# Optimization experiments

Measured on AMD Instinct MI355X. Metric: run time of the kernel, lower is better.

Reference implementation:

```python
import jax, jax.numpy as jnp
import numpy as np

N_NODES = 100_000
N_EDGES = 1_600_000
D = 128  # in = hidden = out channels
LAYERS = 3


def setup_inputs() -> dict:
    key = jax.random.key(0)
    ks = jax.random.split(key, 16)
    inp = {
        "x": jax.random.normal(ks[0], (N_NODES, D), dtype=jnp.float32),
        "edge_weight": jax.random.uniform(ks[1], (N_EDGES,), dtype=jnp.float32),
    }
    scale = 1.0 / np.sqrt(D)
    for l in range(LAYERS):
        inp[f"W_rel_{l}"] = jax.random.normal(ks[2 + 3 * l], (D, D), dtype=jnp.float32) * scale
        inp[f"W_root_{l}"] = jax.random.normal(ks[3 + 3 * l], (D, D), dtype=jnp.float32) * scale
        inp[f"b_{l}"] = jax.random.normal(ks[4 + 3 * l], (D,), dtype=jnp.float32) * scale
    inp["edge_src"] = jax.random.randint(ks[11], (N_EDGES,), 0, N_NODES, dtype=jnp.int32)
    inp["edge_dst"] = jax.random.randint(ks[12], (N_EDGES,), 0, N_NODES, dtype=jnp.int32)
    return inp


def _graph_conv(h, edge_src, edge_dst, edge_weight, W_rel, W_root, b):
    # PyG GraphConv: out_i = W_root @ h_i + W_rel @ (sum_{j->i} w_ji * h_j) + b
    msg = h[edge_src] * edge_weight[:, None]                      # [E, D] gather
    agg = jax.ops.segment_sum(msg, edge_dst, num_segments=h.shape[0])  # [N, D] scatter-add
    return agg @ W_rel.T + h @ W_root.T + b


def reference(x, edge_weight, W_rel_0, W_root_0, b_0, W_rel_1, W_root_1, b_1,
              W_rel_2, W_root_2, b_2, edge_src, edge_dst):
    h = _graph_conv(x, edge_src, edge_dst, edge_weight, W_rel_0, W_root_0, b_0)
    h = jax.nn.relu(h)
    h = _graph_conv(h, edge_src, edge_dst, edge_weight, W_rel_1, W_root_1, b_1)
    h = jax.nn.relu(h)
    h = _graph_conv(h, edge_src, edge_dst, edge_weight, W_rel_2, W_root_2, b_2)
    return h
```

## Files before the change

### kernel.cpp

```cpp
#include <hip/hip_runtime.h>

#define N_NODES 100000
#define N_EDGES 1600000
#define D 128
#define GEMM_GRID 3125
#define BK_NODES 256
#define N_BUCKETS 391
#define BKT_CAP 5120
#define SC_BLOCKS 128
#define EPB 12500

typedef _Float16 f16;
typedef _Float16 f16x8 __attribute__((ext_vector_type(8)));
typedef _Float16 f16x2 __attribute__((ext_vector_type(2)));
typedef float f32x2 __attribute__((ext_vector_type(2)));
typedef float f32x4 __attribute__((ext_vector_type(4)));

__device__ __forceinline__ unsigned bf16bits(float x) {
    unsigned u = __float_as_uint(x);
    return ((u + 0x8000u) >> 16) & 0x7fffu;
}


__global__ __launch_bounds__(256) void bucket_scatter(const int* __restrict__ src,
                                                      const int* __restrict__ dst,
                                                      const float* __restrict__ w,
                                                      int* __restrict__ bcur,
                                                      int2* __restrict__ bkt) {
    __shared__ int hist[N_BUCKETS];
    __shared__ int base[N_BUCKETS];
    int tid = threadIdx.x;
    int v0  = blockIdx.x * (EPB / 4);
    const int4*   dst4 = (const int4*)dst;
    const int4*   src4 = (const int4*)src;
    const float4* w4   = (const float4*)w;

    for (int b = tid; b < N_BUCKETS; b += 256) hist[b] = 0;
    __syncthreads();

    for (int v = tid; v < EPB / 4; v += 256) {
        int4 d = dst4[v0 + v];
        atomicAdd(&hist[d.x >> 8], 1);
        atomicAdd(&hist[d.y >> 8], 1);
        atomicAdd(&hist[d.z >> 8], 1);
        atomicAdd(&hist[d.w >> 8], 1);
    }
    __syncthreads();

    for (int b = tid; b < N_BUCKETS; b += 256) {
        int c = hist[b];
        base[b] = b * BKT_CAP + ((c > 0) ? atomicAdd(&bcur[b], c) : 0);
        hist[b] = 0;
    }
    __syncthreads();

    for (int v = tid; v < EPB / 4; v += 256) {
        int4   d = dst4[v0 + v];
        int4   s = src4[v0 + v];
        float4 f = w4[v0 + v];
        {
            int p = base[d.x >> 8] + atomicAdd(&hist[d.x >> 8], 1);
            bkt[p] = make_int2(s.x, (int)(((unsigned)d.x << 15) | bf16bits(f.x)));
        }
        {
            int p = base[d.y >> 8] + atomicAdd(&hist[d.y >> 8], 1);
            bkt[p] = make_int2(s.y, (int)(((unsigned)d.y << 15) | bf16bits(f.y)));
        }
        {
            int p = base[d.z >> 8] + atomicAdd(&hist[d.z >> 8], 1);
            bkt[p] = make_int2(s.z, (int)(((unsigned)d.z << 15) | bf16bits(f.z)));
        }
        {
            int p = base[d.w >> 8] + atomicAdd(&hist[d.w >> 8], 1);
            bkt[p] = make_int2(s.w, (int)(((unsigned)d.w << 15) | bf16bits(f.w)));
        }
    }
}

__global__ __launch_bounds__(512) void bucket_scan(const int* __restrict__ bcnt,
                                                   int* __restrict__ bbase) {
    __shared__ int sc[512];
    int tid = threadIdx.x;
    int v = (tid < N_BUCKETS) ? bcnt[tid] : 0;
    sc[tid] = v;
    __syncthreads();
    for (int off = 1; off < 512; off <<= 1) {
        int t = (tid >= off) ? sc[tid - off] : 0;
        __syncthreads();
        sc[tid] += t;
        __syncthreads();
    }
    if (tid < N_BUCKETS) bbase[tid] = sc[tid] - v;
}

__global__ __launch_bounds__(256) void bucket_finalize(const int* __restrict__ bcnt,
                                                       const int* __restrict__ bbase,
                                                       const int2* __restrict__ bkt,
                                                       unsigned* __restrict__ csr,
                                                       int* __restrict__ row_ptr) {
    __shared__ int ncnt[BK_NODES];
    __shared__ int noff[BK_NODES];
    __shared__ int sc[BK_NODES];
    int tid   = threadIdx.x;
    int b     = blockIdx.x;
    int node0 = b * BK_NODES;
    int cnt   = bcnt[b];
    int base  = bbase[b];
    int e0    = b * BKT_CAP;

    ncnt[tid] = 0;
    __syncthreads();
    for (int i = tid; i < cnt; i += 256) {
        int local = (int)((unsigned)bkt[e0 + i].y >> 15) - node0;
        atomicAdd(&ncnt[local], 1);
    }
    __syncthreads();
    int s = ncnt[tid];
    sc[tid] = s;
    __syncthreads();
    for (int off = 1; off < 256; off <<= 1) {
        int t = (tid >= off) ? sc[tid - off] : 0;
        __syncthreads();
        sc[tid] += t;
        __syncthreads();
    }
    noff[tid] = sc[tid] - s;
    ncnt[tid] = 0;
    {
        int nN = N_NODES - node0; if (nN > BK_NODES) nN = BK_NODES;
        if (tid < nN) row_ptr[node0 + tid] = base + noff[tid];
        if (b == N_BUCKETS - 1 && tid == 0) row_ptr[N_NODES] = N_EDGES;
    }
    __syncthreads();
    for (int i = tid; i < cnt; i += 256) {
        int2 t = bkt[e0 + i];
        unsigned meta = (unsigned)t.y;
        int local = (int)(meta >> 15) - node0;
        int p = base + noff[local] + atomicAdd(&ncnt[local], 1);
        csr[p] = ((unsigned)t.x << 15) | (meta & 0x7fffu);
    }
}


__global__ __launch_bounds__(256) void cvt_x(const float* __restrict__ in,
                                             f16* __restrict__ out16,
                                             unsigned char* __restrict__ out8) {
    int i = blockIdx.x * 256 + threadIdx.x;
    const float4* in4 = (const float4*)in;
    float4 a = in4[i * 2], b = in4[i * 2 + 1];
    f16x8 v;
    v[0] = (f16)a.x; v[1] = (f16)a.y; v[2] = (f16)a.z; v[3] = (f16)a.w;
    v[4] = (f16)b.x; v[5] = (f16)b.y; v[6] = (f16)b.z; v[7] = (f16)b.w;
    ((f16x8*)out16)[i] = v;
    uint2 p8;
    int r = __builtin_amdgcn_cvt_pk_fp8_f32(a.x, a.y, 0, false);
    r     = __builtin_amdgcn_cvt_pk_fp8_f32(a.z, a.w, r, true);
    p8.x = (unsigned)r;
    r     = __builtin_amdgcn_cvt_pk_fp8_f32(b.x, b.y, 0, false);
    r     = __builtin_amdgcn_cvt_pk_fp8_f32(b.z, b.w, r, true);
    p8.y = (unsigned)r;
    ((uint2*)out8)[i] = p8;
}


__global__ __launch_bounds__(256) void pack_weights(const float* __restrict__ Wrel,
                                                    const float* __restrict__ Wroot,
                                                    f16* __restrict__ Bp) {
    int idx = blockIdx.x * 256 + threadIdx.x;
    int e = idx & 7, lane = (idx >> 3) & 63, ct = (idx >> 9) & 7, ks = idx >> 12;
    int j = ct * 16 + (lane & 15);
    int k = ks * 32 + (lane >> 4) * 8 + e;
    float w = (k < D) ? Wrel[j * D + k] : Wroot[j * D + (k - D)];
    Bp[idx] = (f16)w;
}


#define FMA8(CWV)                                                              \
    {                                                                          \
        float w = __uint_as_float(((CWV) & 0x7fffu) << 16);                    \
        f32x2 c0 = __builtin_amdgcn_cvt_pk_f32_fp8((int)rv[j].x, false);       \
        f32x2 c1 = __builtin_amdgcn_cvt_pk_f32_fp8((int)rv[j].x, true);        \
        f32x2 c2 = __builtin_amdgcn_cvt_pk_f32_fp8((int)rv[j].y, false);       \
        f32x2 c3 = __builtin_amdgcn_cvt_pk_f32_fp8((int)rv[j].y, true);        \
        a0 = fmaf(w, c0.x, a0); a1 = fmaf(w, c0.y, a1);                        \
        a2 = fmaf(w, c1.x, a2); a3 = fmaf(w, c1.y, a3);                        \
        a4 = fmaf(w, c2.x, a4); a5 = fmaf(w, c2.y, a5);                        \
        a6 = fmaf(w, c3.x, a6); a7 = fmaf(w, c3.y, a7);                        \
    }

template <int FINAL>
__global__ __launch_bounds__(256) void fused_layer(const f16* __restrict__ h,
                                                   const unsigned char* __restrict__ h8,
                                                   const int* __restrict__ row_ptr,
                                                   const unsigned* __restrict__ csr,
                                                   const f16x8* __restrict__ Bp,
                                                   const float* __restrict__ bias,
                                                   void* __restrict__ outp,
                                                   unsigned char* __restrict__ outp8) {
    __shared__ f16 sA[32 * 256];
    int tid  = threadIdx.x;
    int lane = tid & 63;
    int wid  = tid >> 6;
    int node0 = blockIdx.x * 32;
    const uint4* h16 = (const uint4*)h;

    int quad = lane >> 4;
    int ql   = lane & 15;
    unsigned qoff = (unsigned)ql * 8u;

    for (int nn = 0; nn < 2; ++nn) {
        int row  = wid * 8 + quad * 2 + nn;
        int node = node0 + row;
        int beg = row_ptr[node], end = row_ptr[node + 1];

        float a0 = 0.f, a1 = 0.f, a2 = 0.f, a3 = 0.f;
        float a4 = 0.f, a5 = 0.f, a6 = 0.f, a7 = 0.f;

        int e = beg;
        unsigned cw[8];
        if (e + 8 <= end) {
#pragma unroll
            for (int j = 0; j < 8; ++j) cw[j] = csr[e + j];
        }
        while (e + 8 <= end) {
            uint2 rv[8];
            __builtin_amdgcn_sched_barrier(0);
#pragma unroll
            for (int j = 0; j < 8; ++j) {
                unsigned off = ((cw[j] >> 8) & 0xFFFFFF80u) | qoff;
                rv[j] = *(const uint2*)(h8 + off);
            }
            unsigned cwn[8];
            bool more = (e + 16 <= end);
            if (more) {
#pragma unroll
                for (int j = 0; j < 8; ++j) cwn[j] = csr[e + 8 + j];
            }
            __builtin_amdgcn_sched_barrier(0);
#pragma unroll
            for (int j = 0; j < 8; ++j) FMA8(cw[j]);
            if (more) {
#pragma unroll
                for (int j = 0; j < 8; ++j) cw[j] = cwn[j];
            }
            e += 8;
        }
        if (e < end) {
            int rem = end - e;
            int em1 = end - 1;
            unsigned sm[8];
            uint2 rv[8];
#pragma unroll
            for (int j = 0; j < 8; ++j) {
                int idx = e + j; idx = idx < em1 ? idx : em1;
                unsigned c = csr[idx];
                sm[j] = (j < rem) ? c : 0u;
            }
            __builtin_amdgcn_sched_barrier(0);
#pragma unroll
            for (int j = 0; j < 8; ++j) {
                unsigned off = ((sm[j] >> 8) & 0xFFFFFF80u) | qoff;
                rv[j] = *(const uint2*)(h8 + off);
            }
            __builtin_amdgcn_sched_barrier(0);
#pragma unroll
            for (int j = 0; j < 8; ++j) FMA8(sm[j]);
        }
        f16x8 ov;
        ov[0] = (f16)a0; ov[1] = (f16)a1; ov[2] = (f16)a2; ov[3] = (f16)a3;
        ov[4] = (f16)a4; ov[5] = (f16)a5; ov[6] = (f16)a6; ov[7] = (f16)a7;
        int o = (row * 256 + ql * 8) ^ ((row & 7) << 3);
        *(f16x8*)&sA[o] = ov;
    }

#pragma unroll
    for (int it = 0; it < 2; ++it) {
        int i = it * 256 + tid, r = i >> 4, c8 = (i & 15) + 16;
        int o = (r * 256 + c8 * 8) ^ ((r & 7) << 3);
        *(uint4*)&sA[o] = h16[(size_t)(node0 + r) * 16 + (c8 - 16)];
    }
    __syncthreads();

    int wrow = wid >> 1;
    int wcol = wid & 1;
    float bv[4];
#pragma unroll
    for (int c = 0; c < 4; ++c) bv[c] = bias[wcol * 64 + c * 16 + (lane & 15)];

    f32x4 acc[4] = {f32x4{0,0,0,0}, f32x4{0,0,0,0}, f32x4{0,0,0,0}, f32x4{0,0,0,0}};
    int arow = wrow * 16 + (lane & 15);
    int kg   = (lane >> 4) * 8;

    f16x8 b0 = Bp[(0 * 8 + wcol * 4 + 0) * 64 + lane];
    f16x8 b1 = Bp[(0 * 8 + wcol * 4 + 1) * 64 + lane];
    f16x8 b2 = Bp[(0 * 8 + wcol * 4 + 2) * 64 + lane];
    f16x8 b3 = Bp[(0 * 8 + wcol * 4 + 3) * 64 + lane];
#pragma unroll 1
    for (int ks = 0; ks < 8; ++ks) {
        f16x8 n0, n1, n2, n3;
        if (ks < 7) {
            n0 = Bp[((ks + 1) * 8 + wcol * 4 + 0) * 64 + lane];
            n1 = Bp[((ks + 1) * 8 + wcol * 4 + 1) * 64 + lane];
            n2 = Bp[((ks + 1) * 8 + wcol * 4 + 2) * 64 + lane];
            n3 = Bp[((ks + 1) * 8 + wcol * 4 + 3) * 64 + lane];
        }
        int o = (arow * 256 + ks * 32 + kg) ^ ((arow & 7) << 3);
        f16x8 afrag = *(const f16x8*)&sA[o];
        acc[0] = __builtin_amdgcn_mfma_f32_16x16x32_f16(afrag, b0, acc[0], 0, 0, 0);
        acc[1] = __builtin_amdgcn_mfma_f32_16x16x32_f16(afrag, b1, acc[1], 0, 0, 0);
        acc[2] = __builtin_amdgcn_mfma_f32_16x16x32_f16(afrag, b2, acc[2], 0, 0, 0);
        acc[3] = __builtin_amdgcn_mfma_f32_16x16x32_f16(afrag, b3, acc[3], 0, 0, 0);
        b0 = n0; b1 = n1; b2 = n2; b3 = n3;
    }

#pragma unroll
    for (int c = 0; c < 4; ++c) {
        int col = wcol * 64 + c * 16 + (lane & 15);
#pragma unroll
        for (int r = 0; r < 4; ++r) {
            int row = node0 + wrow * 16 + (lane >> 4) * 4 + r;
            float o = acc[c][r] + bv[c];
            if (FINAL) {
                ((float*)outp)[(size_t)row * D + col] = o;
            } else {
                o = fmaxf(o, 0.f);
                ((f16*)outp)[(size_t)row * D + col] = (f16)o;
                int pk = __builtin_amdgcn_cvt_pk_fp8_f32(o, o, 0, false);
                outp8[(size_t)row * D + col] = (unsigned char)(pk & 0xff);
            }
        }
    }
}


extern "C" void kernel_launch(void* const* d_in, const int* in_sizes, int n_in,
                              void* d_out, int out_size, void* d_ws, size_t ws_size,
                              hipStream_t stream) {
    const float* x  = (const float*)d_in[0];
    const float* ew = (const float*)d_in[1];
    const float* W_rel[3]  = {(const float*)d_in[2], (const float*)d_in[5], (const float*)d_in[8]};
    const float* W_root[3] = {(const float*)d_in[3], (const float*)d_in[6], (const float*)d_in[9]};
    const float* bias[3]   = {(const float*)d_in[4], (const float*)d_in[7], (const float*)d_in[10]};
    const int* esrc = (const int*)d_in[11];
    const int* edst = (const int*)d_in[12];

    char* ws = (char*)d_ws;
    f16*           bufA16  = (f16*)           (ws);
    unsigned char* bufA8   = (unsigned char*) (ws + 25600000);
    f16*           bufB16  = (f16*)           (ws + 38400000);
    unsigned char* bufB8   = (unsigned char*) (ws + 64000000);
    unsigned*      csr     = (unsigned*)      (ws + 76800000);
    int2*          bkt     = (int2*)          (ws + 83200000);
    int*           row_ptr = (int*)           (ws + 99215360);
    int*           bcur    = (int*)           (ws + 99615376);
    int*           bbase   = (int*)           (ws + 99616940);
    f16*           Bp      = (f16*)           (ws + 99618504);

    hipMemsetAsync(bcur, 0, N_BUCKETS * sizeof(int), stream);
    bucket_scatter<<<SC_BLOCKS, 256, 0, stream>>>(esrc, edst, ew, bcur, bkt);
    bucket_scan<<<1, 512, 0, stream>>>(bcur, bbase);
    bucket_finalize<<<N_BUCKETS, 256, 0, stream>>>(bcur, bbase, bkt, csr, row_ptr);

    cvt_x<<<6250, 256, 0, stream>>>(x, bufA16, bufA8);
    for (int l = 0; l < 3; ++l)
        pack_weights<<<128, 256, 0, stream>>>(W_rel[l], W_root[l], Bp + l * 32768);

    fused_layer<0><<<GEMM_GRID, 256, 0, stream>>>(bufA16, bufA8, row_ptr, csr,
                                                  (const f16x8*)(Bp + 0 * 32768),
                                                  bias[0], bufB16, bufB8);
    fused_layer<0><<<GEMM_GRID, 256, 0, stream>>>(bufB16, bufB8, row_ptr, csr,
                                                  (const f16x8*)(Bp + 1 * 32768),
                                                  bias[1], bufA16, bufA8);
    fused_layer<1><<<GEMM_GRID, 256, 0, stream>>>(bufA16, bufA8, row_ptr, csr,
                                                  (const f16x8*)(Bp + 2 * 32768),
                                                  bias[2], d_out, nullptr);
}
```

Baseline: 226.9 us.

## Halve fused layer tile to 16 nodes per block, doubling grid

```diff
diff --git a/kernel.cpp b/kernel.cpp
--- a/kernel.cpp
+++ b/kernel.cpp
@@ -3,7 +3,8 @@
 #define N_NODES 100000
 #define N_EDGES 1600000
 #define D 128
-#define GEMM_GRID 3125
+#define GEMM_GRID 6250
+#define TILE_ROWS 16
 #define BK_NODES 256
 #define N_BUCKETS 391
 #define BKT_CAP 5120
@@ -197,19 +198,19 @@
                                                    const float* __restrict__ bias,
                                                    void* __restrict__ outp,
                                                    unsigned char* __restrict__ outp8) {
-    __shared__ f16 sA[32 * 256];
+    __shared__ f16 sA[TILE_ROWS * 256];
     int tid  = threadIdx.x;
     int lane = tid & 63;
     int wid  = tid >> 6;
-    int node0 = blockIdx.x * 32;
+    int node0 = blockIdx.x * TILE_ROWS;
     const uint4* h16 = (const uint4*)h;
 
     int quad = lane >> 4;
     int ql   = lane & 15;
     unsigned qoff = (unsigned)ql * 8u;
 
-    for (int nn = 0; nn < 2; ++nn) {
-        int row  = wid * 8 + quad * 2 + nn;
+    {
+        int row  = wid * 4 + quad;
         int node = node0 + row;
         int beg = row_ptr[node], end = row_ptr[node + 1];
 
@@ -273,52 +274,43 @@
         *(f16x8*)&sA[o] = ov;
     }
 
-#pragma unroll
-    for (int it = 0; it < 2; ++it) {
-        int i = it * 256 + tid, r = i >> 4, c8 = (i & 15) + 16;
+    {
+        int r = tid >> 4, c8 = (tid & 15) + 16;
         int o = (r * 256 + c8 * 8) ^ ((r & 7) << 3);
         *(uint4*)&sA[o] = h16[(size_t)(node0 + r) * 16 + (c8 - 16)];
     }
     __syncthreads();
 
-    int wrow = wid >> 1;
-    int wcol = wid & 1;
-    float bv[4];
-#pragma unroll
-    for (int c = 0; c < 4; ++c) bv[c] = bias[wcol * 64 + c * 16 + (lane & 15)];
-
-    f32x4 acc[4] = {f32x4{0,0,0,0}, f32x4{0,0,0,0}, f32x4{0,0,0,0}, f32x4{0,0,0,0}};
-    int arow = wrow * 16 + (lane & 15);
+    float bv[2];
+#pragma unroll
+    for (int c = 0; c < 2; ++c) bv[c] = bias[wid * 32 + c * 16 + (lane & 15)];
+
+    f32x4 acc[2] = {f32x4{0,0,0,0}, f32x4{0,0,0,0}};
+    int arow = lane & 15;
     int kg   = (lane >> 4) * 8;
 
-    f16x8 b0 = Bp[(0 * 8 + wcol * 4 + 0) * 64 + lane];
-    f16x8 b1 = Bp[(0 * 8 + wcol * 4 + 1) * 64 + lane];
-    f16x8 b2 = Bp[(0 * 8 + wcol * 4 + 2) * 64 + lane];
-    f16x8 b3 = Bp[(0 * 8 + wcol * 4 + 3) * 64 + lane];
+    f16x8 b0 = Bp[(0 * 8 + wid * 2 + 0) * 64 + lane];
+    f16x8 b1 = Bp[(0 * 8 + wid * 2 + 1) * 64 + lane];
 #pragma unroll 1
     for (int ks = 0; ks < 8; ++ks) {
-        f16x8 n0, n1, n2, n3;
+        f16x8 n0, n1;
         if (ks < 7) {
-            n0 = Bp[((ks + 1) * 8 + wcol * 4 + 0) * 64 + lane];
-            n1 = Bp[((ks + 1) * 8 + wcol * 4 + 1) * 64 + lane];
-            n2 = Bp[((ks + 1) * 8 + wcol * 4 + 2) * 64 + lane];
-            n3 = Bp[((ks + 1) * 8 + wcol * 4 + 3) * 64 + lane];
+            n0 = Bp[((ks + 1) * 8 + wid * 2 + 0) * 64 + lane];
+            n1 = Bp[((ks + 1) * 8 + wid * 2 + 1) * 64 + lane];
         }
         int o = (arow * 256 + ks * 32 + kg) ^ ((arow & 7) << 3);
         f16x8 afrag = *(const f16x8*)&sA[o];
         acc[0] = __builtin_amdgcn_mfma_f32_16x16x32_f16(afrag, b0, acc[0], 0, 0, 0);
         acc[1] = __builtin_amdgcn_mfma_f32_16x16x32_f16(afrag, b1, acc[1], 0, 0, 0);
-        acc[2] = __builtin_amdgcn_mfma_f32_16x16x32_f16(afrag, b2, acc[2], 0, 0, 0);
-        acc[3] = __builtin_amdgcn_mfma_f32_16x16x32_f16(afrag, b3, acc[3], 0, 0, 0);
-        b0 = n0; b1 = n1; b2 = n2; b3 = n3;
-    }
-
-#pragma unroll
-    for (int c = 0; c < 4; ++c) {
-        int col = wcol * 64 + c * 16 + (lane & 15);
+        b0 = n0; b1 = n1;
+    }
+
+#pragma unroll
+    for (int c = 0; c < 2; ++c) {
+        int col = wid * 32 + c * 16 + (lane & 15);
 #pragma unroll
         for (int r = 0; r < 4; ++r) {
-            int row = node0 + wrow * 16 + (lane >> 4) * 4 + r;
+            int row = node0 + (lane >> 4) * 4 + r;
             float o = acc[c][r] + bv[c];
             if (FINAL) {
                 ((float*)outp)[(size_t)row * D + col] = o;
```

Result: faster. 216.0 us (-4.8%).
